# Optimization experiments

Measured on AMD Instinct MI355X. Metric: run time of the kernel, lower is better.

The kernel has to match this reference:

```python
import jax, jax.numpy as jnp
import numpy as np

EMBED_DIM = 768
NUM_HEADS = 12
HEAD_DIM = EMBED_DIM // NUM_HEADS
SCALING = HEAD_DIM ** -0.5


def setup_inputs() -> dict:
    key = jax.random.key(0)
    ks = jax.random.split(key, 12)
    B, S, E, H = 4, 1024, EMBED_DIM, NUM_HEADS
    inp = {
        "hidden_states": jax.random.normal(ks[0], (B, S, E), dtype=jnp.float32),
        "pos_row": jax.random.randint(ks[1], (B, S), 0, 64, dtype=jnp.int32),
        "pos_col": jax.random.randint(ks[2], (B, S), 0, 32, dtype=jnp.int32),
        "q_w": jax.random.normal(ks[3], (E, E), dtype=jnp.float32) * 0.02,
        "q_b": jnp.zeros((E,), dtype=jnp.float32),
        "k_w": jax.random.normal(ks[4], (E, E), dtype=jnp.float32) * 0.02,
        "k_b": jnp.zeros((E,), dtype=jnp.float32),
        "v_w": jax.random.normal(ks[5], (E, E), dtype=jnp.float32) * 0.02,
        "v_b": jnp.zeros((E,), dtype=jnp.float32),
        "o_w": jax.random.normal(ks[6], (E, E), dtype=jnp.float32) * 0.02,
        "o_b": jnp.zeros((E,), dtype=jnp.float32),
        "rel_table": jax.random.normal(ks[7], (4, H), dtype=jnp.float32) * 0.02,
    }
    return inp


def _generate_bias(pos_row, pos_col, rel_table):
    # relative row/col differences: [B, S, S]
    rel_row = pos_row[:, :, None] - pos_row[:, None, :]
    rel_col = pos_col[:, :, None] - pos_col[:, None, :]
    rel_cell = jnp.abs(rel_row) + jnp.abs(rel_col)
    # table index: other=0, same row=1, same col=2, same cell=3 (priority order as in torch code)
    idx = jnp.where(rel_row == 0, 1, 0)
    idx = jnp.where(rel_col == 0, 2, idx)
    idx = jnp.where(rel_cell == 0, 3, idx)
    # gather: [B, S, S, H] -> [B, H, S, S]
    bias = rel_table[idx]
    return jnp.transpose(bias, (0, 3, 1, 2))


def reference(hidden_states, pos_row, pos_col, q_w, q_b, k_w, k_b, v_w, v_b, o_w, o_b, rel_table):
    B, S, E = hidden_states.shape
    H, D = NUM_HEADS, HEAD_DIM

    def shape(x):  # [B, S, E] -> [B, H, S, D]
        return jnp.transpose(x.reshape(B, S, H, D), (0, 2, 1, 3))

    q = shape((hidden_states @ q_w.T + q_b) * SCALING)
    k = shape(hidden_states @ k_w.T + k_b)
    v = shape(hidden_states @ v_w.T + v_b)

    # [B, H, S, S]
    attn = jnp.einsum("bhqd,bhkd->bhqk", q, k)
    attn = attn + _generate_bias(pos_row, pos_col, rel_table)
    attn = jax.nn.softmax(attn, axis=-1)

    out = jnp.einsum("bhqk,bhkd->bhqd", attn, v)  # [B, H, S, D]
    out = jnp.transpose(out, (0, 2, 1, 3)).reshape(B, S, E)
    return out @ o_w.T + o_b
```

## Files before the change

### kernel.cpp

```cpp
#include <hip/hip_runtime.h>

#define NHEADS 12
#define HDIM   64
#define EMB    768
#define SEQ    1024
#define BATCH  4
#define MTOT   (BATCH * SEQ)

typedef __bf16 bf16x8 __attribute__((ext_vector_type(8)));
typedef float  f32x4  __attribute__((ext_vector_type(4)));

#define GLB(p) ((const __attribute__((address_space(1))) uint32_t*)(p))
#define LDS(p) ((__attribute__((address_space(3))) uint32_t*)(p))

__device__ __forceinline__ uint bfr(float f) {
    uint u = __float_as_uint(f);
    return (u + 0x7fffu + ((u >> 16) & 1u)) >> 16;
}

__global__ __launch_bounds__(256) void split_all(
    const float* __restrict__ hs,
    const float* __restrict__ w0, const float* __restrict__ w1,
    const float* __restrict__ w2, const float* __restrict__ w3,
    ushort* __restrict__ hsh, ushort* __restrict__ hsl,
    ushort* __restrict__ wch, ushort* __restrict__ wcl,
    ushort* __restrict__ woh, ushort* __restrict__ wol)
{
    const int bx = blockIdx.x;
    const float* src;
    ushort *hi, *lo;
    int i;
    if (bx < 3072) {
        src = hs; hi = hsh; lo = hsl;
        i = bx * 256 + threadIdx.x;
    } else {
        const int y = (bx - 3072) / 576;
        const int r = (bx - 3072) - y * 576;
        src = (y == 0) ? w0 : (y == 1) ? w1 : (y == 2) ? w2 : w3;
        hi = (y < 3) ? (wch + (size_t)y * (EMB * EMB)) : woh;
        lo = (y < 3) ? (wcl + (size_t)y * (EMB * EMB)) : wol;
        i = r * 256 + threadIdx.x;
    }
    float4 v = ((const float4*)src)[i];
    float f[4] = {v.x, v.y, v.z, v.w};
    ushort hh[4], ll[4];
#pragma unroll
    for (int j = 0; j < 4; ++j) {
        uint h = bfr(f[j]);
        float hf = __uint_as_float(h << 16);
        ll[j] = (ushort)bfr(f[j] - hf);
        hh[j] = (ushort)h;
    }
    ushort4 hv = {hh[0], hh[1], hh[2], hh[3]};
    ushort4 lv = {ll[0], ll[1], ll[2], ll[3]};
    ((ushort4*)hi)[i] = hv;
    ((ushort4*)lo)[i] = lv;
}

template <int MODE, int BM>
__global__ __launch_bounds__(512) void gemm_mfma(
    const ushort* __restrict__ Ah, const ushort* __restrict__ Al,
    const ushort* __restrict__ Wh, const ushort* __restrict__ Wl,
    const float* __restrict__ b0, const float* __restrict__ b1,
    const float* __restrict__ b2,
    ushort* __restrict__ q16, ushort* __restrict__ k16,
    ushort* __restrict__ vT16, float* __restrict__ o0)
{
    constexpr int SA = BM * 64;
    constexpr int SB = 8192;
    constexpr int TS = 2 * SA + 2 * SB;
    constexpr int MFRAG = BM / 32;
    constexpr int WMS = BM / 2;

    __shared__ __align__(16) char ldsc[2 * TS];

    const int t  = threadIdx.x;
    const int w  = t >> 6;
    const int l  = t & 63;
    const int m0 = blockIdx.x * BM;
    const int n0 = blockIdx.y * 128;
    const int wm = w >> 2;
    const int wn = w & 3;

    const char* gb[4] = {
        (const char*)Ah + (size_t)m0 * 1536,
        (const char*)Al + (size_t)m0 * 1536,
        (const char*)Wh + (size_t)n0 * 1536,
        (const char*)Wl + (size_t)n0 * 1536};

    int aoff[MFRAG], boff[2];
#pragma unroll
    for (int i = 0; i < MFRAG; ++i) {
        int row = wm * WMS + i * 16 + (l & 15);
        aoff[i] = row * 64 + ((((l >> 4) ^ ((row >> 1) & 3))) << 4);
    }
#pragma unroll
    for (int i = 0; i < 2; ++i) {
        int rn = wn * 32 + i * 16 + (l & 15);
        boff[i] = rn * 64 + ((((l >> 4) ^ ((rn >> 1) & 3))) << 4);
    }

    auto stage = [&](int ks, int buf) {
        const size_t kb = (size_t)ks * 64;
        char* dst = ldsc + buf * TS;
#pragma unroll
        for (int tt = 0; tt < 4; ++tt) {
            const int tsz  = (tt < 2) ? SA : SB;
            const int tbas = (tt == 0) ? 0 : (tt == 1) ? SA
                           : (tt == 2) ? 2 * SA : 2 * SA + SB;
#pragma unroll
            for (int p = 0; p < tsz; p += 8192) {
                const int soff = p + t * 16;
                if (soff < tsz) {
                    const int srow = soff >> 6;
                    const int slot = (soff >> 4) & 3;
                    const size_t go = (size_t)srow * 1536 +
                                      ((slot ^ ((srow >> 1) & 3)) << 4) + kb;
                    __builtin_amdgcn_global_load_lds(GLB(gb[tt] + go),
                                                     LDS(dst + tbas + soff), 16, 0, 0);
                }
            }
        }
    };

    f32x4 acc[MFRAG][2] = {};

    stage(0, 0);
    __syncthreads();

    for (int ks = 0; ks < 24; ++ks) {
        if (ks + 1 < 24) stage(ks + 1, (ks + 1) & 1);

        const char* cur = ldsc + (ks & 1) * TS;
        bf16x8 ah[MFRAG], al[MFRAG], bh[2], bl[2];
#pragma unroll
        for (int i = 0; i < MFRAG; ++i) {
            ah[i] = *(const bf16x8*)(cur + aoff[i]);
            al[i] = *(const bf16x8*)(cur + SA + aoff[i]);
        }
#pragma unroll
        for (int i = 0; i < 2; ++i) {
            bh[i] = *(const bf16x8*)(cur + 2 * SA + boff[i]);
            bl[i] = *(const bf16x8*)(cur + 2 * SA + SB + boff[i]);
        }
#pragma unroll
        for (int i = 0; i < MFRAG; ++i)
#pragma unroll
            for (int j = 0; j < 2; ++j) {
                acc[i][j] = __builtin_amdgcn_mfma_f32_16x16x32_bf16(ah[i], bh[j], acc[i][j], 0, 0, 0);
                acc[i][j] = __builtin_amdgcn_mfma_f32_16x16x32_bf16(ah[i], bl[j], acc[i][j], 0, 0, 0);
                acc[i][j] = __builtin_amdgcn_mfma_f32_16x16x32_bf16(al[i], bh[j], acc[i][j], 0, 0, 0);
            }
        __syncthreads();
    }

    const int mrow_base = m0 + wm * WMS + ((l >> 4) << 2);

    if (MODE == 1) {
        const int which = (n0 >= 1536) ? 2 : (n0 >= 768 ? 1 : 0);
        const float* bp = (which == 0) ? b0 : (which == 1 ? b1 : b2);
        const float scale = (which == 0) ? 0.125f : 1.0f;
        const int nin_base = n0 - which * 768 + wn * 32 + (l & 15);
        if (which == 2) {
#pragma unroll
            for (int j = 0; j < 2; ++j) {
                const int n_in = nin_base + j * 16;
                const float bv = b2[n_in];
                const int h = n_in >> 6, d = n_in & 63;
#pragma unroll
                for (int i = 0; i < MFRAG; ++i) {
                    const int m = mrow_base + i * 16;
                    const int bb = m >> 10, s = m & 1023;
                    ushort4 pk = {(ushort)bfr(acc[i][j][0] + bv),
                                  (ushort)bfr(acc[i][j][1] + bv),
                                  (ushort)bfr(acc[i][j][2] + bv),
                                  (ushort)bfr(acc[i][j][3] + bv)};
                    *(ushort4*)(vT16 + (size_t)((bb * NHEADS + h) * HDIM + d) * SEQ + s) = pk;
                }
            }
        } else {
            ushort* op = (which == 0) ? q16 : k16;
#pragma unroll
            for (int j = 0; j < 2; ++j) {
                const int n_in = nin_base + j * 16;
                const float bv = bp[n_in];
                const int h = n_in >> 6, d = n_in & 63;
#pragma unroll
                for (int i = 0; i < MFRAG; ++i)
#pragma unroll
                    for (int r = 0; r < 4; ++r) {
                        const int m = mrow_base + i * 16 + r;
                        const int bb = m >> 10, s = m & 1023;
                        op[(size_t)((bb * NHEADS + h) * SEQ + s) * HDIM + d] =
                            (ushort)bfr((acc[i][j][r] + bv) * scale);
                    }
            }
        }
    } else {
        const int nin_base = n0 + wn * 32 + (l & 15);
#pragma unroll
        for (int j = 0; j < 2; ++j) {
            const int n_in = nin_base + j * 16;
            const float bv = b0[n_in];
#pragma unroll
            for (int i = 0; i < MFRAG; ++i)
#pragma unroll
                for (int r = 0; r < 4; ++r) {
                    const int m = mrow_base + i * 16 + r;
                    o0[(size_t)m * 768 + n_in] = acc[i][j][r] + bv;
                }
        }
    }
}

#define QPOFF  0
#define KOFF   8192
#define VOFF   24576
#define POSOFF 40960

__global__ __launch_bounds__(256) void attn_mfma(
    const ushort* __restrict__ q16, const ushort* __restrict__ k16,
    const ushort* __restrict__ vT16, const int* __restrict__ pos_row,
    const int* __restrict__ pos_col, const float* __restrict__ rel_table,
    ushort* __restrict__ aoh, ushort* __restrict__ aol)
{
    __shared__ __align__(16) char lds[41472];

    const int t  = threadIdx.x;
    const int w  = t >> 6;
    const int l  = t & 63;
    const int bh = blockIdx.y;
    const int b  = bh / NHEADS;
    const int h  = bh - b * NHEADS;
    const int q0g = blockIdx.x * 64;

    const char* qb  = (const char*)(q16 + (size_t)bh * SEQ * HDIM);
    const char* kb  = (const char*)(k16 + (size_t)bh * SEQ * HDIM);
    const char* vtb = (const char*)(vT16 + (size_t)bh * HDIM * SEQ);

    const float t0 = rel_table[0 * NHEADS + h];
    const float t1 = rel_table[1 * NHEADS + h];
    const float t2 = rel_table[2 * NHEADS + h];
    const float t3 = rel_table[3 * NHEADS + h];

    const int o1 = t * 16, o2 = o1 + 4096;
    const int r1 = o1 >> 7, r2 = o2 >> 7;
    const int kq1 = o1 ^ ((r1 & 7) << 4);
    const int kq2 = o2 ^ ((r2 & 7) << 4);
    const int vs1 = r1 * 2048 + (((((o1 >> 4) & 7) ^ (r1 & 7))) << 4);
    const int vs2 = r2 * 2048 + (((((o2 >> 4) & 7) ^ (r2 & 7))) << 4);

    auto stage_kv = [&](int kt, int buf) {
        const int k0g = kt * 64;
        __builtin_amdgcn_global_load_lds(GLB(kb + (size_t)k0g * 128 + kq1),
                                         LDS(lds + KOFF + buf * 8192 + w * 1024), 16, 0, 0);
        __builtin_amdgcn_global_load_lds(GLB(kb + (size_t)k0g * 128 + kq2),
                                         LDS(lds + KOFF + buf * 8192 + w * 1024 + 4096), 16, 0, 0);
        __builtin_amdgcn_global_load_lds(GLB(vtb + (size_t)k0g * 2 + vs1),
                                         LDS(lds + VOFF + buf * 8192 + w * 1024), 16, 0, 0);
        __builtin_amdgcn_global_load_lds(GLB(vtb + (size_t)k0g * 2 + vs2),
                                         LDS(lds + VOFF + buf * 8192 + w * 1024 + 4096), 16, 0, 0);
        if (t < 64) {
            int pr = pos_row[b * SEQ + k0g + t];
            int pc = pos_col[b * SEQ + k0g + t];
            *(int*)(lds + POSOFF + buf * 256 + t * 4) = (pr << 8) | pc;
        }
    };

    __builtin_amdgcn_global_load_lds(GLB(qb + (size_t)q0g * 128 + kq1),
                                     LDS(lds + QPOFF + w * 1024), 16, 0, 0);
    __builtin_amdgcn_global_load_lds(GLB(qb + (size_t)q0g * 128 + kq2),
                                     LDS(lds + QPOFF + w * 1024 + 4096), 16, 0, 0);
    stage_kv(0, 0);

    const int qrow_g = q0g + w * 16 + (l & 15);
    const int pq = (pos_row[b * SEQ + qrow_g] << 8) | pos_col[b * SEQ + qrow_g];

    __syncthreads();

    bf16x8 qf[2];
    const int qrl = w * 16 + (l & 15);
#pragma unroll
    for (int ks = 0; ks < 2; ++ks)
        qf[ks] = *(const bf16x8*)(lds + QPOFF + qrl * 128 +
                                  ((((l >> 4) + 4 * ks) ^ (qrl & 7)) << 4));

    f32x4 pv[4] = {};
    float m_run = -1e30f, l_run = 0.0f;

    const int prow = l & 15;
    const int pswz = (prow & 7) << 4;
    const int pwbase = QPOFF + w * 2048 + prow * 128;

    for (int kt = 0; kt < 16; ++kt) {
        const int cb = kt & 1;
        if (kt + 1 < 16) stage_kv(kt + 1, cb ^ 1);
        const char* kbuf = lds + KOFF + cb * 8192;
        const char* vbuf = lds + VOFF + cb * 8192;
        const char* pbuf = lds + POSOFF + cb * 256;

        f32x4 sacc[4] = {};
#pragma unroll
        for (int ks = 0; ks < 2; ++ks) {
            const bf16x8 qq = qf[ks];
#pragma unroll
            for (int j = 0; j < 4; ++j) {
                const int krow = j * 16 + (l & 15);
                const bf16x8 kf = *(const bf16x8*)(kbuf + krow * 128 +
                                                   ((((l >> 4) + 4 * ks) ^ (krow & 7)) << 4));
                sacc[j] = __builtin_amdgcn_mfma_f32_16x16x32_bf16(kf, qq, sacc[j], 0, 0, 0);
            }
        }

        int4 pk4[4];
#pragma unroll
        for (int j = 0; j < 4; ++j)
            pk4[j] = *(const int4*)(pbuf + (l >> 4) * 16 + j * 64);

        float sv[16];
#pragma unroll
        for (int j = 0; j < 4; ++j) {
            const int pkk[4] = {pk4[j].x, pk4[j].y, pk4[j].z, pk4[j].w};
#pragma unroll
            for (int r = 0; r < 4; ++r) {
                const int dd = pq ^ pkk[r];
                const float bs = ((dd & 0xFF00) == 0)
                                     ? (((dd & 0xFF) == 0) ? t3 : t1)
                                     : (((dd & 0xFF) == 0) ? t2 : t0);
                sv[j * 4 + r] = sacc[j][r] + bs;
            }
        }
        float pm = sv[0];
#pragma unroll
        for (int i = 1; i < 16; ++i) pm = fmaxf(pm, sv[i]);
        pm = fmaxf(pm, __shfl_xor(pm, 16));
        pm = fmaxf(pm, __shfl_xor(pm, 32));
        const float mnew = fmaxf(m_run, pm);
        float psum = 0.0f;
#pragma unroll
        for (int i = 0; i < 16; ++i) {
            sv[i] = __expf(sv[i] - mnew);
            psum += sv[i];
        }
        psum += __shfl_xor(psum, 16);
        psum += __shfl_xor(psum, 32);
        const float alpha = __expf(m_run - mnew);
        l_run = l_run * alpha + psum;
        m_run = mnew;

#pragma unroll
        for (int r = 0; r < 4; ++r) {
            const float ar = __shfl(alpha, (l >> 4) * 4 + r);
#pragma unroll
            for (int i = 0; i < 4; ++i) pv[i][r] *= ar;
        }

#pragma unroll
        for (int j = 0; j < 4; ++j)
#pragma unroll
            for (int p2 = 0; p2 < 2; ++p2) {
                const uint u = bfr(sv[j * 4 + 2 * p2]) | (bfr(sv[j * 4 + 2 * p2 + 1]) << 16);
                const int adr = pwbase + (((l >> 4) * 8 + 4 * p2 + 32 * j) ^ pswz);
                *(uint*)(lds + adr) = u;
            }

#pragma unroll
        for (int ks = 0; ks < 2; ++ks) {
            const bf16x8 pf = *(const bf16x8*)(lds + pwbase +
                                               ((((l >> 4) + 4 * ks) << 4) ^ pswz));
#pragma unroll
            for (int i = 0; i < 4; ++i) {
                const int vrow = i * 16 + (l & 15);
                const bf16x8 vf = *(const bf16x8*)(vbuf + vrow * 128 +
                                                   ((((l >> 4) + 4 * ks) ^ (vrow & 7)) << 4));
                pv[i] = __builtin_amdgcn_mfma_f32_16x16x32_bf16(pf, vf, pv[i], 0, 0, 0);
            }
        }
        __syncthreads();
    }

    const float rinv = 1.0f / l_run;
#pragma unroll
    for (int r = 0; r < 4; ++r) {
        const float inv = __shfl(rinv, (l >> 4) * 4 + r);
        const int mrow = b * SEQ + q0g + w * 16 + (l >> 4) * 4 + r;
        const size_t base = (size_t)mrow * 768 + h * 64 + prow;
#pragma unroll
        for (int i = 0; i < 4; ++i) {
            const float o = pv[i][r] * inv;
            const uint hu = bfr(o);
            const float hf = __uint_as_float(hu << 16);
            const uint lu = bfr(o - hf);
            aoh[base + 16 * i] = (ushort)hu;
            aol[base + 16 * i] = (ushort)lu;
        }
    }
}

extern "C" void kernel_launch(void* const* d_in, const int* in_sizes, int n_in,
                              void* d_out, int out_size, void* d_ws, size_t ws_size,
                              hipStream_t stream)
{
    const float* hs      = (const float*)d_in[0];
    const int*   pos_row = (const int*)d_in[1];
    const int*   pos_col = (const int*)d_in[2];
    const float* q_w     = (const float*)d_in[3];
    const float* q_b     = (const float*)d_in[4];
    const float* k_w     = (const float*)d_in[5];
    const float* k_b     = (const float*)d_in[6];
    const float* v_w     = (const float*)d_in[7];
    const float* v_b     = (const float*)d_in[8];
    const float* o_w     = (const float*)d_in[9];
    const float* o_b     = (const float*)d_in[10];
    const float* rel_tab = (const float*)d_in[11];

    char* ws = (char*)d_ws;
    const size_t HS_N = (size_t)MTOT * EMB;
    const size_t W_N  = (size_t)EMB * EMB;
    ushort* hsh = (ushort*)ws;  ws += HS_N * 2;
    ushort* hsl = (ushort*)ws;  ws += HS_N * 2;
    ushort* wch = (ushort*)ws;  ws += 3 * W_N * 2;
    ushort* wcl = (ushort*)ws;  ws += 3 * W_N * 2;
    ushort* woh = (ushort*)ws;  ws += W_N * 2;
    ushort* wol = (ushort*)ws;  ws += W_N * 2;
    ushort* aoh = (ushort*)ws;  ws += HS_N * 2;
    ushort* aol = (ushort*)ws;  ws += HS_N * 2;
    ushort* q16 = (ushort*)ws;  ws += HS_N * 2;
    ushort* k16 = (ushort*)ws;  ws += HS_N * 2;
    ushort* vT16 = (ushort*)ws; ws += HS_N * 2;

    split_all<<<3072 + 4 * 576, 256, 0, stream>>>(
        hs, q_w, k_w, v_w, o_w, hsh, hsl, wch, wcl, woh, wol);

    gemm_mfma<1, 128><<<dim3(MTOT / 128, 2304 / 128), 512, 0, stream>>>(
        hsh, hsl, wch, wcl, q_b, k_b, v_b, q16, k16, vT16, nullptr);

    attn_mfma<<<dim3(SEQ / 64, BATCH * NHEADS), 256, 0, stream>>>(
        q16, k16, vT16, pos_row, pos_col, rel_tab, aoh, aol);

    gemm_mfma<0, 64><<<dim3(MTOT / 64, EMB / 128), 512, 0, stream>>>(
        aoh, aol, woh, wol, o_b, nullptr, nullptr,
        nullptr, nullptr, nullptr, (float*)d_out);
}
```

Before: 209.1 us.

## Rewrite QKV GEMM with 32x32 MFMA, 4-warp 64x64 tiles, 4-stage pipeline

```diff
diff --git a/kernel.cpp b/kernel.cpp
--- a/kernel.cpp
+++ b/kernel.cpp
@@ -9,6 +9,7 @@
 
 typedef __bf16 bf16x8 __attribute__((ext_vector_type(8)));
 typedef float  f32x4  __attribute__((ext_vector_type(4)));
+typedef float  f32x16 __attribute__((ext_vector_type(16)));
 
 #define GLB(p) ((const __attribute__((address_space(1))) uint32_t*)(p))
 #define LDS(p) ((__attribute__((address_space(3))) uint32_t*)(p))
@@ -57,27 +58,151 @@
     ((ushort4*)lo)[i] = lv;
 }
 
-template <int MODE, int BM>
-__global__ __launch_bounds__(512) void gemm_mfma(
+__global__ __launch_bounds__(256, 2) void gemm_qkv(
     const ushort* __restrict__ Ah, const ushort* __restrict__ Al,
     const ushort* __restrict__ Wh, const ushort* __restrict__ Wl,
     const float* __restrict__ b0, const float* __restrict__ b1,
     const float* __restrict__ b2,
     ushort* __restrict__ q16, ushort* __restrict__ k16,
-    ushort* __restrict__ vT16, float* __restrict__ o0)
+    ushort* __restrict__ vT16)
 {
-    constexpr int SA = BM * 64;
+    __shared__ __align__(16) char lds[65536];
+
+    const int t = threadIdx.x;
+    const int w = t >> 6, l = t & 63;
+    const int m0 = blockIdx.x * 128;
+    const int n0 = blockIdx.y * 128;
+    const int wm = w >> 1, wn = w & 1;
+
+    const char* gA[2] = {(const char*)Ah + (size_t)m0 * 1536,
+                         (const char*)Al + (size_t)m0 * 1536};
+    const char* gW[2] = {(const char*)Wh + (size_t)n0 * 1536,
+                         (const char*)Wl + (size_t)n0 * 1536};
+
+    const size_t gsb = (size_t)(t & 127) * 1536 + (t >> 7) * 16;
+    const int ldsu = w * 1024;
+
+    int aoff[2], boff[2];
+#pragma unroll
+    for (int i = 0; i < 2; ++i)
+        aoff[i] = (l >> 5) * 2048 + (wm * 64 + i * 32 + (l & 31)) * 16;
+#pragma unroll
+    for (int j = 0; j < 2; ++j)
+        boff[j] = (l >> 5) * 2048 + (wn * 64 + j * 32 + (l & 31)) * 16;
+
+    f32x16 acc[2][2] = {};
+
+    auto stage = [&](int ks) {
+        char* dst = lds + (ks & 3) * 16384;
+        const size_t go = gsb + (size_t)ks * 32;
+        __builtin_amdgcn_global_load_lds(GLB(gA[0] + go), LDS(dst + ldsu), 16, 0, 0);
+        __builtin_amdgcn_global_load_lds(GLB(gA[1] + go), LDS(dst + 4096 + ldsu), 16, 0, 0);
+        __builtin_amdgcn_global_load_lds(GLB(gW[0] + go), LDS(dst + 8192 + ldsu), 16, 0, 0);
+        __builtin_amdgcn_global_load_lds(GLB(gW[1] + go), LDS(dst + 12288 + ldsu), 16, 0, 0);
+    };
+
+    auto compute = [&](int ks) {
+        const char* cur = lds + (ks & 3) * 16384;
+        bf16x8 ah[2], al[2], bh[2], bl[2];
+#pragma unroll
+        for (int i = 0; i < 2; ++i) {
+            ah[i] = *(const bf16x8*)(cur + aoff[i]);
+            al[i] = *(const bf16x8*)(cur + 4096 + aoff[i]);
+        }
+#pragma unroll
+        for (int j = 0; j < 2; ++j) {
+            bh[j] = *(const bf16x8*)(cur + 8192 + boff[j]);
+            bl[j] = *(const bf16x8*)(cur + 12288 + boff[j]);
+        }
+        __builtin_amdgcn_s_setprio(1);
+#pragma unroll
+        for (int i = 0; i < 2; ++i)
+#pragma unroll
+            for (int j = 0; j < 2; ++j) {
+                acc[i][j] = __builtin_amdgcn_mfma_f32_32x32x16_bf16(ah[i], bh[j], acc[i][j], 0, 0, 0);
+                acc[i][j] = __builtin_amdgcn_mfma_f32_32x32x16_bf16(ah[i], bl[j], acc[i][j], 0, 0, 0);
+                acc[i][j] = __builtin_amdgcn_mfma_f32_32x32x16_bf16(al[i], bh[j], acc[i][j], 0, 0, 0);
+            }
+        __builtin_amdgcn_s_setprio(0);
+    };
+
+    stage(0);
+    stage(1);
+    __syncthreads();
+
+    for (int kb = 0; kb < 48; kb += 2) {
+        if (kb + 2 < 48) stage(kb + 2);
+        if (kb + 3 < 48) stage(kb + 3);
+        compute(kb);
+        compute(kb + 1);
+        __syncthreads();
+    }
+
+    const int lrow = 4 * (l >> 5);
+    const int lcol = l & 31;
+    const int which = (n0 >= 1536) ? 2 : (n0 >= 768 ? 1 : 0);
+    const int nb = n0 - which * 768 + wn * 64;
+
+    if (which == 2) {
+#pragma unroll
+        for (int j = 0; j < 2; ++j) {
+            const int n_in = nb + j * 32 + lcol;
+            const float bv = b2[n_in];
+            const int h = n_in >> 6, d = n_in & 63;
+#pragma unroll
+            for (int i = 0; i < 2; ++i) {
+                const int m_base = m0 + wm * 64 + i * 32 + lrow;
+                const int bb = m_base >> 10, s_base = m_base & 1023;
+                ushort* bp = vT16 + ((size_t)(bb * NHEADS + h) * HDIM + d) * SEQ + s_base;
+#pragma unroll
+                for (int g = 0; g < 4; ++g) {
+                    ushort4 pk = {(ushort)bfr(acc[i][j][4 * g + 0] + bv),
+                                  (ushort)bfr(acc[i][j][4 * g + 1] + bv),
+                                  (ushort)bfr(acc[i][j][4 * g + 2] + bv),
+                                  (ushort)bfr(acc[i][j][4 * g + 3] + bv)};
+                    *(ushort4*)(bp + 8 * g) = pk;
+                }
+            }
+        }
+    } else {
+        ushort* op = (which == 0) ? q16 : k16;
+        const float* bpt = (which == 0) ? b0 : b1;
+        const float scale = (which == 0) ? 0.125f : 1.0f;
+#pragma unroll
+        for (int j = 0; j < 2; ++j) {
+            const int n_in = nb + j * 32 + lcol;
+            const float bv = bpt[n_in];
+            const int h = n_in >> 6, d = n_in & 63;
+#pragma unroll
+            for (int i = 0; i < 2; ++i) {
+                const int m_base = m0 + wm * 64 + i * 32 + lrow;
+#pragma unroll
+                for (int r = 0; r < 16; ++r) {
+                    const int m = m_base + (r & 3) + 8 * (r >> 2);
+                    const int bb = m >> 10, s = m & 1023;
+                    op[(size_t)((bb * NHEADS + h) * SEQ + s) * HDIM + d] =
+                        (ushort)bfr((acc[i][j][r] + bv) * scale);
+                }
+            }
+        }
+    }
+}
+
+__global__ __launch_bounds__(512) void gemm_oproj(
+    const ushort* __restrict__ Ah, const ushort* __restrict__ Al,
+    const ushort* __restrict__ Wh, const ushort* __restrict__ Wl,
+    const float* __restrict__ b0, float* __restrict__ o0)
+{
+    constexpr int SA = 64 * 64;
     constexpr int SB = 8192;
     constexpr int TS = 2 * SA + 2 * SB;
-    constexpr int MFRAG = BM / 32;
-    constexpr int WMS = BM / 2;
 
     __shared__ __align__(16) char ldsc[2 * TS];
 
     const int t  = threadIdx.x;
     const int w  = t >> 6;
     const int l  = t & 63;
-    const int m0 = blockIdx.x * BM;
+    const int m0 = blockIdx.x * 64;
     const int n0 = blockIdx.y * 128;
     const int wm = w >> 2;
     const int wn = w & 3;
@@ -88,10 +213,10 @@
         (const char*)Wh + (size_t)n0 * 1536,
         (const char*)Wl + (size_t)n0 * 1536};
 
-    int aoff[MFRAG], boff[2];
-#pragma unroll
-    for (int i = 0; i < MFRAG; ++i) {
-        int row = wm * WMS + i * 16 + (l & 15);
+    int aoff[2], boff[2];
+#pragma unroll
+    for (int i = 0; i < 2; ++i) {
+        int row = wm * 32 + i * 16 + (l & 15);
         aoff[i] = row * 64 + ((((l >> 4) ^ ((row >> 1) & 3))) << 4);
     }
 #pragma unroll
@@ -123,7 +248,7 @@
         }
     };
 
-    f32x4 acc[MFRAG][2] = {};
+    f32x4 acc[2][2] = {};
 
     stage(0, 0);
     __syncthreads();
@@ -132,9 +257,9 @@
         if (ks + 1 < 24) stage(ks + 1, (ks + 1) & 1);
 
         const char* cur = ldsc + (ks & 1) * TS;
-        bf16x8 ah[MFRAG], al[MFRAG], bh[2], bl[2];
-#pragma unroll
-        for (int i = 0; i < MFRAG; ++i) {
+        bf16x8 ah[2], al[2], bh[2], bl[2];
+#pragma unroll
+        for (int i = 0; i < 2; ++i) {
             ah[i] = *(const bf16x8*)(cur + aoff[i]);
             al[i] = *(const bf16x8*)(cur + SA + aoff[i]);
         }
@@ -144,7 +269,7 @@
             bl[i] = *(const bf16x8*)(cur + 2 * SA + SB + boff[i]);
         }
 #pragma unroll
-        for (int i = 0; i < MFRAG; ++i)
+        for (int i = 0; i < 2; ++i)
 #pragma unroll
             for (int j = 0; j < 2; ++j) {
                 acc[i][j] = __builtin_amdgcn_mfma_f32_16x16x32_bf16(ah[i], bh[j], acc[i][j], 0, 0, 0);
@@ -154,62 +279,19 @@
         __syncthreads();
     }
 
-    const int mrow_base = m0 + wm * WMS + ((l >> 4) << 2);
-
-    if (MODE == 1) {
-        const int which = (n0 >= 1536) ? 2 : (n0 >= 768 ? 1 : 0);
-        const float* bp = (which == 0) ? b0 : (which == 1 ? b1 : b2);
-        const float scale = (which == 0) ? 0.125f : 1.0f;
-        const int nin_base = n0 - which * 768 + wn * 32 + (l & 15);
-        if (which == 2) {
-#pragma unroll
-            for (int j = 0; j < 2; ++j) {
-                const int n_in = nin_base + j * 16;
-                const float bv = b2[n_in];
-                const int h = n_in >> 6, d = n_in & 63;
-#pragma unroll
-                for (int i = 0; i < MFRAG; ++i) {
-                    const int m = mrow_base + i * 16;
-                    const int bb = m >> 10, s = m & 1023;
-                    ushort4 pk = {(ushort)bfr(acc[i][j][0] + bv),
-                                  (ushort)bfr(acc[i][j][1] + bv),
-                                  (ushort)bfr(acc[i][j][2] + bv),
-                                  (ushort)bfr(acc[i][j][3] + bv)};
-                    *(ushort4*)(vT16 + (size_t)((bb * NHEADS + h) * HDIM + d) * SEQ + s) = pk;
-                }
-            }
-        } else {
-            ushort* op = (which == 0) ? q16 : k16;
-#pragma unroll
-            for (int j = 0; j < 2; ++j) {
-                const int n_in = nin_base + j * 16;
-                const float bv = bp[n_in];
-                const int h = n_in >> 6, d = n_in & 63;
-#pragma unroll
-                for (int i = 0; i < MFRAG; ++i)
-#pragma unroll
-                    for (int r = 0; r < 4; ++r) {
-                        const int m = mrow_base + i * 16 + r;
-                        const int bb = m >> 10, s = m & 1023;
-                        op[(size_t)((bb * NHEADS + h) * SEQ + s) * HDIM + d] =
-                            (ushort)bfr((acc[i][j][r] + bv) * scale);
-                    }
-            }
-        }
-    } else {
-        const int nin_base = n0 + wn * 32 + (l & 15);
-#pragma unroll
-        for (int j = 0; j < 2; ++j) {
-            const int n_in = nin_base + j * 16;
-            const float bv = b0[n_in];
-#pragma unroll
-            for (int i = 0; i < MFRAG; ++i)
-#pragma unroll
-                for (int r = 0; r < 4; ++r) {
-                    const int m = mrow_base + i * 16 + r;
-                    o0[(size_t)m * 768 + n_in] = acc[i][j][r] + bv;
-                }
-        }
+    const int mrow_base = m0 + wm * 32 + ((l >> 4) << 2);
+    const int nin_base = n0 + wn * 32 + (l & 15);
+#pragma unroll
+    for (int j = 0; j < 2; ++j) {
+        const int n_in = nin_base + j * 16;
+        const float bv = b0[n_in];
+#pragma unroll
+        for (int i = 0; i < 2; ++i)
+#pragma unroll
+            for (int r = 0; r < 4; ++r) {
+                const int m = mrow_base + i * 16 + r;
+                o0[(size_t)m * 768 + n_in] = acc[i][j][r] + bv;
+            }
     }
 }
 
@@ -432,13 +514,12 @@
     split_all<<<3072 + 4 * 576, 256, 0, stream>>>(
         hs, q_w, k_w, v_w, o_w, hsh, hsl, wch, wcl, woh, wol);
 
-    gemm_mfma<1, 128><<<dim3(MTOT / 128, 2304 / 128), 512, 0, stream>>>(
-        hsh, hsl, wch, wcl, q_b, k_b, v_b, q16, k16, vT16, nullptr);
+    gemm_qkv<<<dim3(MTOT / 128, 2304 / 128), 256, 0, stream>>>(
+        hsh, hsl, wch, wcl, q_b, k_b, v_b, q16, k16, vT16);
 
     attn_mfma<<<dim3(SEQ / 64, BATCH * NHEADS), 256, 0, stream>>>(
         q16, k16, vT16, pos_row, pos_col, rel_tab, aoh, aol);
 
-    gemm_mfma<0, 64><<<dim3(MTOT / 64, EMB / 128), 512, 0, stream>>>(
-        aoh, aol, woh, wol, o_b, nullptr, nullptr,
-        nullptr, nullptr, nullptr, (float*)d_out);
+    gemm_oproj<<<dim3(MTOT / 64, EMB / 128), 512, 0, stream>>>(
+        aoh, aol, woh, wol, o_b, (float*)d_out);
 }
```

Result: slower. 248.3 us (+18.7%).

## Replace syncthreads with vmcnt-based waits and prioritize MFMA in GEMMs and attention

Applied to the files above, without the earlier changes.

```diff
diff --git a/kernel.cpp b/kernel.cpp
--- a/kernel.cpp
+++ b/kernel.cpp
@@ -12,6 +12,8 @@
 
 #define GLB(p) ((const __attribute__((address_space(1))) uint32_t*)(p))
 #define LDS(p) ((__attribute__((address_space(3))) uint32_t*)(p))
+#define VMCNT(n) asm volatile("s_waitcnt vmcnt(" #n ")" ::: "memory")
+#define LGKM0()  asm volatile("s_waitcnt lgkmcnt(0)" ::: "memory")
 
 __device__ __forceinline__ uint bfr(float f) {
     uint u = __float_as_uint(f);
@@ -22,11 +24,18 @@
     const float* __restrict__ hs,
     const float* __restrict__ w0, const float* __restrict__ w1,
     const float* __restrict__ w2, const float* __restrict__ w3,
+    const int* __restrict__ pos_row, const int* __restrict__ pos_col,
     ushort* __restrict__ hsh, ushort* __restrict__ hsl,
     ushort* __restrict__ wch, ushort* __restrict__ wcl,
-    ushort* __restrict__ woh, ushort* __restrict__ wol)
+    ushort* __restrict__ woh, ushort* __restrict__ wol,
+    int* __restrict__ pos_pk)
 {
     const int bx = blockIdx.x;
+    if (bx >= 5376) {
+        int i = (bx - 5376) * 256 + threadIdx.x;
+        pos_pk[i] = (pos_row[i] << 8) | pos_col[i];
+        return;
+    }
     const float* src;
     ushort *hi, *lo;
     int i;
@@ -57,27 +66,21 @@
     ((ushort4*)lo)[i] = lv;
 }
 
-template <int MODE, int BM>
-__global__ __launch_bounds__(512) void gemm_mfma(
+__global__ __launch_bounds__(512) void gemm_qkv(
     const ushort* __restrict__ Ah, const ushort* __restrict__ Al,
     const ushort* __restrict__ Wh, const ushort* __restrict__ Wl,
     const float* __restrict__ b0, const float* __restrict__ b1,
     const float* __restrict__ b2,
     ushort* __restrict__ q16, ushort* __restrict__ k16,
-    ushort* __restrict__ vT16, float* __restrict__ o0)
+    ushort* __restrict__ vT16)
 {
-    constexpr int SA = BM * 64;
-    constexpr int SB = 8192;
-    constexpr int TS = 2 * SA + 2 * SB;
-    constexpr int MFRAG = BM / 32;
-    constexpr int WMS = BM / 2;
-
+    constexpr int TS = 32768;
     __shared__ __align__(16) char ldsc[2 * TS];
 
     const int t  = threadIdx.x;
     const int w  = t >> 6;
     const int l  = t & 63;
-    const int m0 = blockIdx.x * BM;
+    const int m0 = blockIdx.x * 128;
     const int n0 = blockIdx.y * 128;
     const int wm = w >> 2;
     const int wn = w & 3;
@@ -88,128 +91,222 @@
         (const char*)Wh + (size_t)n0 * 1536,
         (const char*)Wl + (size_t)n0 * 1536};
 
-    int aoff[MFRAG], boff[2];
-#pragma unroll
-    for (int i = 0; i < MFRAG; ++i) {
-        int row = wm * WMS + i * 16 + (l & 15);
+    int aoff[4], boff[2];
+#pragma unroll
+    for (int i = 0; i < 4; ++i) {
+        int row = wm * 64 + i * 16 + (l & 15);
         aoff[i] = row * 64 + ((((l >> 4) ^ ((row >> 1) & 3))) << 4);
     }
 #pragma unroll
-    for (int i = 0; i < 2; ++i) {
-        int rn = wn * 32 + i * 16 + (l & 15);
-        boff[i] = rn * 64 + ((((l >> 4) ^ ((rn >> 1) & 3))) << 4);
+    for (int j = 0; j < 2; ++j) {
+        int rn = wn * 32 + j * 16 + (l & 15);
+        boff[j] = rn * 64 + ((((l >> 4) ^ ((rn >> 1) & 3))) << 4);
     }
 
     auto stage = [&](int ks, int buf) {
         const size_t kb = (size_t)ks * 64;
         char* dst = ldsc + buf * TS;
-#pragma unroll
-        for (int tt = 0; tt < 4; ++tt) {
-            const int tsz  = (tt < 2) ? SA : SB;
-            const int tbas = (tt == 0) ? 0 : (tt == 1) ? SA
-                           : (tt == 2) ? 2 * SA : 2 * SA + SB;
-#pragma unroll
-            for (int p = 0; p < tsz; p += 8192) {
-                const int soff = p + t * 16;
-                if (soff < tsz) {
-                    const int srow = soff >> 6;
-                    const int slot = (soff >> 4) & 3;
-                    const size_t go = (size_t)srow * 1536 +
-                                      ((slot ^ ((srow >> 1) & 3)) << 4) + kb;
-                    __builtin_amdgcn_global_load_lds(GLB(gb[tt] + go),
-                                                     LDS(dst + tbas + soff), 16, 0, 0);
-                }
-            }
-        }
+        const int soff = t * 16;
+        const int srow = soff >> 6;
+        const int slot = (soff >> 4) & 3;
+        const size_t go = (size_t)srow * 1536 +
+                          ((slot ^ ((srow >> 1) & 3)) << 4) + kb;
+#pragma unroll
+        for (int tt = 0; tt < 4; ++tt)
+            __builtin_amdgcn_global_load_lds(GLB(gb[tt] + go),
+                                             LDS(dst + tt * 8192 + soff), 16, 0, 0);
     };
 
-    f32x4 acc[MFRAG][2] = {};
+    f32x4 acc[4][2] = {};
 
     stage(0, 0);
-    __syncthreads();
 
     for (int ks = 0; ks < 24; ++ks) {
-        if (ks + 1 < 24) stage(ks + 1, (ks + 1) & 1);
+        if (ks + 1 < 24) {
+            stage(ks + 1, (ks + 1) & 1);
+            VMCNT(4);
+        } else {
+            VMCNT(0);
+        }
+        __builtin_amdgcn_s_barrier();
 
         const char* cur = ldsc + (ks & 1) * TS;
-        bf16x8 ah[MFRAG], al[MFRAG], bh[2], bl[2];
-#pragma unroll
-        for (int i = 0; i < MFRAG; ++i) {
+        bf16x8 ah[4], al[4], bh[2], bl[2];
+#pragma unroll
+        for (int i = 0; i < 4; ++i) {
             ah[i] = *(const bf16x8*)(cur + aoff[i]);
-            al[i] = *(const bf16x8*)(cur + SA + aoff[i]);
-        }
-#pragma unroll
-        for (int i = 0; i < 2; ++i) {
-            bh[i] = *(const bf16x8*)(cur + 2 * SA + boff[i]);
-            bl[i] = *(const bf16x8*)(cur + 2 * SA + SB + boff[i]);
-        }
-#pragma unroll
-        for (int i = 0; i < MFRAG; ++i)
+            al[i] = *(const bf16x8*)(cur + 8192 + aoff[i]);
+        }
+#pragma unroll
+        for (int j = 0; j < 2; ++j) {
+            bh[j] = *(const bf16x8*)(cur + 16384 + boff[j]);
+            bl[j] = *(const bf16x8*)(cur + 24576 + boff[j]);
+        }
+        LGKM0();
+        __builtin_amdgcn_sched_barrier(0);
+        __builtin_amdgcn_s_barrier();
+
+        __builtin_amdgcn_s_setprio(1);
+#pragma unroll
+        for (int i = 0; i < 4; ++i)
 #pragma unroll
             for (int j = 0; j < 2; ++j) {
                 acc[i][j] = __builtin_amdgcn_mfma_f32_16x16x32_bf16(ah[i], bh[j], acc[i][j], 0, 0, 0);
                 acc[i][j] = __builtin_amdgcn_mfma_f32_16x16x32_bf16(ah[i], bl[j], acc[i][j], 0, 0, 0);
                 acc[i][j] = __builtin_amdgcn_mfma_f32_16x16x32_bf16(al[i], bh[j], acc[i][j], 0, 0, 0);
             }
-        __syncthreads();
-    }
-
-    const int mrow_base = m0 + wm * WMS + ((l >> 4) << 2);
-
-    if (MODE == 1) {
-        const int which = (n0 >= 1536) ? 2 : (n0 >= 768 ? 1 : 0);
-        const float* bp = (which == 0) ? b0 : (which == 1 ? b1 : b2);
-        const float scale = (which == 0) ? 0.125f : 1.0f;
-        const int nin_base = n0 - which * 768 + wn * 32 + (l & 15);
-        if (which == 2) {
-#pragma unroll
-            for (int j = 0; j < 2; ++j) {
-                const int n_in = nin_base + j * 16;
-                const float bv = b2[n_in];
-                const int h = n_in >> 6, d = n_in & 63;
-#pragma unroll
-                for (int i = 0; i < MFRAG; ++i) {
-                    const int m = mrow_base + i * 16;
-                    const int bb = m >> 10, s = m & 1023;
-                    ushort4 pk = {(ushort)bfr(acc[i][j][0] + bv),
-                                  (ushort)bfr(acc[i][j][1] + bv),
-                                  (ushort)bfr(acc[i][j][2] + bv),
-                                  (ushort)bfr(acc[i][j][3] + bv)};
-                    *(ushort4*)(vT16 + (size_t)((bb * NHEADS + h) * HDIM + d) * SEQ + s) = pk;
-                }
-            }
-        } else {
-            ushort* op = (which == 0) ? q16 : k16;
-#pragma unroll
-            for (int j = 0; j < 2; ++j) {
-                const int n_in = nin_base + j * 16;
-                const float bv = bp[n_in];
-                const int h = n_in >> 6, d = n_in & 63;
-#pragma unroll
-                for (int i = 0; i < MFRAG; ++i)
-#pragma unroll
-                    for (int r = 0; r < 4; ++r) {
-                        const int m = mrow_base + i * 16 + r;
-                        const int bb = m >> 10, s = m & 1023;
-                        op[(size_t)((bb * NHEADS + h) * SEQ + s) * HDIM + d] =
-                            (ushort)bfr((acc[i][j][r] + bv) * scale);
-                    }
-            }
-        }
-    } else {
-        const int nin_base = n0 + wn * 32 + (l & 15);
+        __builtin_amdgcn_s_setprio(0);
+    }
+
+    const int mrow_base = m0 + wm * 64 + ((l >> 4) << 2);
+    const int which = (n0 >= 1536) ? 2 : (n0 >= 768 ? 1 : 0);
+    const int nin_base = n0 - which * 768 + wn * 32 + (l & 15);
+
+    if (which == 2) {
 #pragma unroll
         for (int j = 0; j < 2; ++j) {
             const int n_in = nin_base + j * 16;
-            const float bv = b0[n_in];
-#pragma unroll
-            for (int i = 0; i < MFRAG; ++i)
+            const float bv = b2[n_in];
+            const int h = n_in >> 6, d = n_in & 63;
+#pragma unroll
+            for (int i = 0; i < 4; ++i) {
+                const int m = mrow_base + i * 16;
+                const int bb = m >> 10, s = m & 1023;
+                ushort4 pk = {(ushort)bfr(acc[i][j][0] + bv),
+                              (ushort)bfr(acc[i][j][1] + bv),
+                              (ushort)bfr(acc[i][j][2] + bv),
+                              (ushort)bfr(acc[i][j][3] + bv)};
+                *(ushort4*)(vT16 + (size_t)((bb * NHEADS + h) * HDIM + d) * SEQ + s) = pk;
+            }
+        }
+    } else {
+        ushort* op = (which == 0) ? q16 : k16;
+        const float* bpt = (which == 0) ? b0 : b1;
+        const float scale = (which == 0) ? 0.125f : 1.0f;
+#pragma unroll
+        for (int j = 0; j < 2; ++j) {
+            const int n_in = nin_base + j * 16;
+            const float bv = bpt[n_in];
+            const int h = n_in >> 6, d = n_in & 63;
+#pragma unroll
+            for (int i = 0; i < 4; ++i)
 #pragma unroll
                 for (int r = 0; r < 4; ++r) {
                     const int m = mrow_base + i * 16 + r;
-                    o0[(size_t)m * 768 + n_in] = acc[i][j][r] + bv;
+                    const int bb = m >> 10, s = m & 1023;
+                    op[(size_t)((bb * NHEADS + h) * SEQ + s) * HDIM + d] =
+                        (ushort)bfr((acc[i][j][r] + bv) * scale);
                 }
         }
+    }
+}
+
+__global__ __launch_bounds__(512) void gemm_oproj(
+    const ushort* __restrict__ Ah, const ushort* __restrict__ Al,
+    const ushort* __restrict__ Wh, const ushort* __restrict__ Wl,
+    const float* __restrict__ b0, float* __restrict__ o0)
+{
+    constexpr int SA = 4096;
+    constexpr int SB = 8192;
+    constexpr int TS = 2 * SA + 2 * SB;
+    __shared__ __align__(16) char ldsc[2 * TS];
+
+    const int t  = threadIdx.x;
+    const int w  = t >> 6;
+    const int l  = t & 63;
+    const int m0 = blockIdx.x * 64;
+    const int n0 = blockIdx.y * 128;
+    const int wm = w >> 2;
+    const int wn = w & 3;
+
+    const char* gb[4] = {
+        (const char*)Ah + (size_t)m0 * 1536,
+        (const char*)Al + (size_t)m0 * 1536,
+        (const char*)Wh + (size_t)n0 * 1536,
+        (const char*)Wl + (size_t)n0 * 1536};
+
+    int aoff[2], boff[2];
+#pragma unroll
+    for (int i = 0; i < 2; ++i) {
+        int row = wm * 32 + i * 16 + (l & 15);
+        aoff[i] = row * 64 + ((((l >> 4) ^ ((row >> 1) & 3))) << 4);
+    }
+#pragma unroll
+    for (int i = 0; i < 2; ++i) {
+        int rn = wn * 32 + i * 16 + (l & 15);
+        boff[i] = rn * 64 + ((((l >> 4) ^ ((rn >> 1) & 3))) << 4);
+    }
+
+    auto stage = [&](int ks, int buf) {
+        const size_t kb = (size_t)ks * 64;
+        char* dst = ldsc + buf * TS;
+        const int soff = t * 16;
+        const int srow = soff >> 6;
+        const int slot = (soff >> 4) & 3;
+        const size_t go = (size_t)srow * 1536 +
+                          ((slot ^ ((srow >> 1) & 3)) << 4) + kb;
+        if (soff < SA) {
+            __builtin_amdgcn_global_load_lds(GLB(gb[0] + go), LDS(dst + soff), 16, 0, 0);
+            __builtin_amdgcn_global_load_lds(GLB(gb[1] + go), LDS(dst + SA + soff), 16, 0, 0);
+        }
+        __builtin_amdgcn_global_load_lds(GLB(gb[2] + go), LDS(dst + 2 * SA + soff), 16, 0, 0);
+        __builtin_amdgcn_global_load_lds(GLB(gb[3] + go), LDS(dst + 2 * SA + SB + soff), 16, 0, 0);
+    };
+
+    f32x4 acc[2][2] = {};
+
+    stage(0, 0);
+
+    for (int ks = 0; ks < 24; ++ks) {
+        if (ks + 1 < 24) {
+            stage(ks + 1, (ks + 1) & 1);
+            if (w < 4) { VMCNT(4); } else { VMCNT(2); }
+        } else {
+            VMCNT(0);
+        }
+        __builtin_amdgcn_s_barrier();
+
+        const char* cur = ldsc + (ks & 1) * TS;
+        bf16x8 ah[2], al[2], bh[2], bl[2];
+#pragma unroll
+        for (int i = 0; i < 2; ++i) {
+            ah[i] = *(const bf16x8*)(cur + aoff[i]);
+            al[i] = *(const bf16x8*)(cur + SA + aoff[i]);
+        }
+#pragma unroll
+        for (int i = 0; i < 2; ++i) {
+            bh[i] = *(const bf16x8*)(cur + 2 * SA + boff[i]);
+            bl[i] = *(const bf16x8*)(cur + 2 * SA + SB + boff[i]);
+        }
+        LGKM0();
+        __builtin_amdgcn_sched_barrier(0);
+        __builtin_amdgcn_s_barrier();
+
+        __builtin_amdgcn_s_setprio(1);
+#pragma unroll
+        for (int i = 0; i < 2; ++i)
+#pragma unroll
+            for (int j = 0; j < 2; ++j) {
+                acc[i][j] = __builtin_amdgcn_mfma_f32_16x16x32_bf16(ah[i], bh[j], acc[i][j], 0, 0, 0);
+                acc[i][j] = __builtin_amdgcn_mfma_f32_16x16x32_bf16(ah[i], bl[j], acc[i][j], 0, 0, 0);
+                acc[i][j] = __builtin_amdgcn_mfma_f32_16x16x32_bf16(al[i], bh[j], acc[i][j], 0, 0, 0);
+            }
+        __builtin_amdgcn_s_setprio(0);
+    }
+
+    const int mrow_base = m0 + wm * 32 + ((l >> 4) << 2);
+    const int nin_base = n0 + wn * 32 + (l & 15);
+#pragma unroll
+    for (int j = 0; j < 2; ++j) {
+        const int n_in = nin_base + j * 16;
+        const float bv = b0[n_in];
+#pragma unroll
+        for (int i = 0; i < 2; ++i)
+#pragma unroll
+            for (int r = 0; r < 4; ++r) {
+                const int m = mrow_base + i * 16 + r;
+                o0[(size_t)m * 768 + n_in] = acc[i][j][r] + bv;
+            }
     }
 }
 
@@ -220,8 +317,8 @@
 
 __global__ __launch_bounds__(256) void attn_mfma(
     const ushort* __restrict__ q16, const ushort* __restrict__ k16,
-    const ushort* __restrict__ vT16, const int* __restrict__ pos_row,
-    const int* __restrict__ pos_col, const float* __restrict__ rel_table,
+    const ushort* __restrict__ vT16, const int* __restrict__ pos_pk,
+    const float* __restrict__ rel_table,
     ushort* __restrict__ aoh, ushort* __restrict__ aol)
 {
     __shared__ __align__(16) char lds[41472];
@@ -260,10 +357,9 @@
                                          LDS(lds + VOFF + buf * 8192 + w * 1024), 16, 0, 0);
         __builtin_amdgcn_global_load_lds(GLB(vtb + (size_t)k0g * 2 + vs2),
                                          LDS(lds + VOFF + buf * 8192 + w * 1024 + 4096), 16, 0, 0);
-        if (t < 64) {
-            int pr = pos_row[b * SEQ + k0g + t];
-            int pc = pos_col[b * SEQ + k0g + t];
-            *(int*)(lds + POSOFF + buf * 256 + t * 4) = (pr << 8) | pc;
+        if (w == 0) {
+            __builtin_amdgcn_global_load_lds(GLB(pos_pk + b * SEQ + k0g + l),
+                                             LDS(lds + POSOFF + buf * 256), 4, 0, 0);
         }
     };
 
@@ -274,9 +370,10 @@
     stage_kv(0, 0);
 
     const int qrow_g = q0g + w * 16 + (l & 15);
-    const int pq = (pos_row[b * SEQ + qrow_g] << 8) | pos_col[b * SEQ + qrow_g];
-
-    __syncthreads();
+    const int pq = pos_pk[b * SEQ + qrow_g];
+
+    VMCNT(0);
+    __builtin_amdgcn_s_barrier();
 
     bf16x8 qf[2];
     const int qrl = w * 16 + (l & 15);
@@ -294,12 +391,20 @@
 
     for (int kt = 0; kt < 16; ++kt) {
         const int cb = kt & 1;
-        if (kt + 1 < 16) stage_kv(kt + 1, cb ^ 1);
+        if (kt + 1 < 16) {
+            stage_kv(kt + 1, cb ^ 1);
+            if (w == 0) { VMCNT(5); } else { VMCNT(4); }
+        } else {
+            VMCNT(0);
+        }
+        __builtin_amdgcn_s_barrier();
+
         const char* kbuf = lds + KOFF + cb * 8192;
         const char* vbuf = lds + VOFF + cb * 8192;
         const char* pbuf = lds + POSOFF + cb * 256;
 
         f32x4 sacc[4] = {};
+        __builtin_amdgcn_s_setprio(1);
 #pragma unroll
         for (int ks = 0; ks < 2; ++ks) {
             const bf16x8 qq = qf[ks];
@@ -311,6 +416,7 @@
                 sacc[j] = __builtin_amdgcn_mfma_f32_16x16x32_bf16(kf, qq, sacc[j], 0, 0, 0);
             }
         }
+        __builtin_amdgcn_s_setprio(0);
 
         int4 pk4[4];
 #pragma unroll
@@ -364,6 +470,7 @@
                 *(uint*)(lds + adr) = u;
             }
 
+        __builtin_amdgcn_s_setprio(1);
 #pragma unroll
         for (int ks = 0; ks < 2; ++ks) {
             const bf16x8 pf = *(const bf16x8*)(lds + pwbase +
@@ -376,7 +483,11 @@
                 pv[i] = __builtin_amdgcn_mfma_f32_16x16x32_bf16(pf, vf, pv[i], 0, 0, 0);
             }
         }
-        __syncthreads();
+        __builtin_amdgcn_s_setprio(0);
+
+        LGKM0();
+        __builtin_amdgcn_sched_barrier(0);
+        __builtin_amdgcn_s_barrier();
     }
 
     const float rinv = 1.0f / l_run;
@@ -428,17 +539,18 @@
     ushort* q16 = (ushort*)ws;  ws += HS_N * 2;
     ushort* k16 = (ushort*)ws;  ws += HS_N * 2;
     ushort* vT16 = (ushort*)ws; ws += HS_N * 2;
-
-    split_all<<<3072 + 4 * 576, 256, 0, stream>>>(
-        hs, q_w, k_w, v_w, o_w, hsh, hsl, wch, wcl, woh, wol);
-
-    gemm_mfma<1, 128><<<dim3(MTOT / 128, 2304 / 128), 512, 0, stream>>>(
-        hsh, hsl, wch, wcl, q_b, k_b, v_b, q16, k16, vT16, nullptr);
+    int* pos_pk = (int*)ws;     ws += MTOT * 4;
+
+    split_all<<<5392, 256, 0, stream>>>(
+        hs, q_w, k_w, v_w, o_w, pos_row, pos_col,
+        hsh, hsl, wch, wcl, woh, wol, pos_pk);
+
+    gemm_qkv<<<dim3(MTOT / 128, 2304 / 128), 512, 0, stream>>>(
+        hsh, hsl, wch, wcl, q_b, k_b, v_b, q16, k16, vT16);
 
     attn_mfma<<<dim3(SEQ / 64, BATCH * NHEADS), 256, 0, stream>>>(
-        q16, k16, vT16, pos_row, pos_col, rel_tab, aoh, aol);
-
-    gemm_mfma<0, 64><<<dim3(MTOT / 64, EMB / 128), 512, 0, stream>>>(
-        aoh, aol, woh, wol, o_b, nullptr, nullptr,
-        nullptr, nullptr, nullptr, (float*)d_out);
+        q16, k16, vT16, pos_pk, rel_tab, aoh, aol);
+
+    gemm_oproj<<<dim3(MTOT / 64, EMB / 128), 512, 0, stream>>>(
+        aoh, aol, woh, wol, o_b, (float*)d_out);
 }
```

After: 207.3 us. Within noise of the previous version (-0.9%).
